# Kernel tuning notes

Measured on AMD Instinct MI355X. Metric: run time of the kernel, lower is better.

Reference implementation:

```python
import jax, jax.numpy as jnp
import numpy as np

LMAX = 6
BLOCK_SIZES = [(2 * l + 1) ** 2 for l in range(LMAX + 1)]  # [1,9,25,49,81,121,169], sum=455
IRREPS_DIM = sum(BLOCK_SIZES)


def setup_inputs() -> dict:
    key = jax.random.key(0)
    k1, k2, k3 = jax.random.split(key, 3)
    B, F_IN, F_OUT, N_GRID = 256, 128, 128, 512
    x = jax.random.normal(k1, (B, F_IN, IRREPS_DIM), dtype=jnp.float32)
    w = jax.random.normal(k2, (F_IN, F_OUT, N_GRID), dtype=jnp.float32)
    D = jax.random.normal(k3, (N_GRID, IRREPS_DIM), dtype=jnp.float32)
    return {"x": x, "w": w, "D": D}


def _so3_linear(x, psi):
    # x: [B, f_in, 455], psi: [f_in, f_out, 455]
    # Per-degree grouped linear: for each l, input block is (mul=2l+1, dim=2l+1),
    # weight block is (mul_in=2l+1, mul_out=2l+1); e3nn normalization 1/sqrt(f_in*mul_in).
    B, f_in, _ = x.shape
    f_out = psi.shape[1]
    outs = []
    off = 0
    for l in range(LMAX + 1):
        d = 2 * l + 1
        sz = d * d
        xb = x[:, :, off:off + sz].reshape(B, f_in, d, d)          # [B,f,u,i]
        wb = psi[:, :, off:off + sz].reshape(f_in, f_out, d, d)    # [f,g,u,v]
        yb = jnp.einsum('bfui,fguv->bgvi', xb, wb) / np.sqrt(f_in * d).astype(np.float32)
        outs.append(yb.reshape(B, f_out, sz))
        off += sz
    return jnp.concatenate(outs, axis=-1)  # [B, f_out, 455]


def reference(x, w, D):
    n_grid = D.shape[0]
    # Kernel synthesis from Wigner-D buffer: psi[f,g,i] = sum_n D[n,i] * w[f,g,n] / sqrt(n_grid)
    psi = jnp.einsum('ni,xyn->xyi', D, w) / np.float32(np.sqrt(n_grid))
    return _so3_linear(x, psi)
```

## Files before the change

### kernel.cpp

```cpp
#include <hip/hip_runtime.h>
#include <math.h>


typedef float f32x4 __attribute__((ext_vector_type(4)));
typedef short short8 __attribute__((ext_vector_type(8)));
typedef short short4v __attribute__((ext_vector_type(4)));
typedef __bf16 bf8 __attribute__((ext_vector_type(8)));

static __device__ inline bf8 as_bf8(short8 s) {
    union { short8 s; bf8 b; } u; u.s = s; return u.b;
}
static __device__ inline short f2bf(float f) {
    union { float f; unsigned u; } v; v.f = f;
    unsigned r = v.u + 0x7FFFu + ((v.u >> 16) & 1u);
    return (short)(r >> 16);
}
static __device__ __forceinline__ void glds16(const short* g, short* l) {
    __builtin_amdgcn_global_load_lds(
        (const __attribute__((address_space(1))) unsigned*)g,
        (__attribute__((address_space(3))) unsigned*)l, 16, 0, 0);
}

static const int OFFS_H[8] = {0, 1, 10, 35, 84, 165, 286, 455};
static const size_t PSIOFF_H[7] = {0, 16384, 163840, 573440, 1376256, 2703360, 4685824};
static const size_t XPOFF_H[7] = {0, 32768, 327680, 1146880, 2752512, 5406720, 9371648};
__constant__ int OFFS_D[8] = {0, 1, 10, 35, 84, 165, 286, 455};
__constant__ unsigned PSIOFF_D[7] = {0, 16384, 163840, 573440, 1376256, 2703360, 4685824};
__constant__ unsigned XPOFF_D[7] = {0, 32768, 327680, 1146880, 2752512, 5406720, 9371648};
__constant__ int PSTART2_D[7] = {0, 338, 580, 742, 840, 890, 908};

__global__ void transpose_D(const float* __restrict__ D, short* __restrict__ DT) {
    int idx = blockIdx.x * 256 + threadIdx.x;
    if (idx >= 455 * 512) return;
    int n = idx & 511, c = idx >> 9;
    DT[(size_t)c * 512 + n] = f2bf(D[(size_t)n * 455 + c]);
}

static __device__ __forceinline__ void psi_body(int rawid, const float* __restrict__ w,
                                                const short* __restrict__ DT,
                                                short* __restrict__ PSIall,
                                                short (*As)[72], short (*Bs)[72],
                                                int* colInfo) {
    int id = (rawid & 7) * 128 + (rawid >> 3);
    const int nt = id & 3, mt = id >> 2;
    const int tid = threadIdx.x, wave = tid >> 6, lane = tid & 63;
    const int wm = (wave & 1) * 32, wn = (wave >> 1) * 64;

    if (tid < 128) {
        int cp = nt * 128 + tid;
        int info = -1;
        if (cp < 455) {
            int l = 6;
            while (OFFS_D[l] > cp) --l;
            int t = cp - OFFS_D[l];
            int d = 2 * l + 1;
            int v = t / d, u = t - v * d;
            info = (OFFS_D[l] + u * d + v) | (u << 9) | (v << 13) | (l << 17);
        }
        colInfo[tid] = info;
    }
    __syncthreads();

    int brow[4];
#pragma unroll
    for (int c = 0; c < 4; ++c) {
        int inf = colInfo[(tid + c * 256) >> 3];
        brow[c] = (inf < 0) ? 0 : (inf & 511);
    }

    const float* Ag = w + (size_t)(mt * 64) * 512;
    f32x4 acc[2][4] = {};

    for (int k0 = 0; k0 < 512; k0 += 64) {
        __syncthreads();
#pragma unroll
        for (int c = 0; c < 4; ++c) {
            int e = (tid + c * 256) * 4;
            int r = e >> 6, cc = e & 63;
            float4 v = *reinterpret_cast<const float4*>(Ag + (size_t)r * 512 + k0 + cc);
            short4v s;
            s.x = f2bf(v.x); s.y = f2bf(v.y); s.z = f2bf(v.z); s.w = f2bf(v.w);
            *reinterpret_cast<short4v*>(&As[r][cc]) = s;
        }
#pragma unroll
        for (int c = 0; c < 4; ++c) {
            int ch = tid + c * 256;
            int r = ch >> 3, cc = (ch & 7) * 8;
            short8 v = *reinterpret_cast<const short8*>(DT + (size_t)brow[c] * 512 + k0 + cc);
            *reinterpret_cast<short8*>(&Bs[r][cc]) = v;
        }
        __syncthreads();
#pragma unroll
        for (int kf = 0; kf < 2; ++kf) {
            const int kc = kf * 32 + (lane >> 4) * 8;
            short8 af[2], bfr[4];
#pragma unroll
            for (int mi = 0; mi < 2; ++mi)
                af[mi] = *reinterpret_cast<const short8*>(&As[wm + mi * 16 + (lane & 15)][kc]);
#pragma unroll
            for (int ni = 0; ni < 4; ++ni)
                bfr[ni] = *reinterpret_cast<const short8*>(&Bs[wn + ni * 16 + (lane & 15)][kc]);
#pragma unroll
            for (int mi = 0; mi < 2; ++mi)
#pragma unroll
                for (int ni = 0; ni < 4; ++ni)
                    acc[mi][ni] = __builtin_amdgcn_mfma_f32_16x16x32_bf16(
                        as_bf8(af[mi]), as_bf8(bfr[ni]), acc[mi][ni], 0, 0, 0);
        }
    }

    const float s1 = 0.044194173824159216f;
    const int f = mt >> 1;
#pragma unroll
    for (int mi = 0; mi < 2; ++mi)
#pragma unroll
        for (int ni = 0; ni < 4; ++ni) {
            int inf = colInfo[wn + ni * 16 + (lane & 15)];
            if (inf >= 0) {
                int u = (inf >> 9) & 15, v = (inf >> 13) & 15, l = (inf >> 17) & 7;
                int d = 2 * l + 1;
                size_t base = PSIOFF_D[l];
#pragma unroll
                for (int r = 0; r < 4; ++r) {
                    int m = mt * 64 + wm + mi * 16 + (lane >> 4) * 4 + r;
                    int g = m & 127;
                    PSIall[base + (size_t)(g * d + v) * (128 * d) + f * d + u] =
                        f2bf(acc[mi][ni][r] * s1);
                }
            }
        }
}

static __device__ __forceinline__ void pack_body(int id, const float* __restrict__ x,
                                                 short* __restrict__ XPall,
                                                 short (*Ls)[170]) {
    const int l = 6 - (id >> 10);
    const int local = id & 1023;
    const int fc = local & 3, b = local >> 2;
    const int d = 2 * l + 1, sz = d * d, off = OFFS_D[l];
    const int K = 128 * d;

    const int tid = threadIdx.x;
    const float* xb = x + ((size_t)b * 128 + fc * 32) * 455 + off;
    const int total = 32 * sz;
    for (int e = tid; e < total; e += 256) {
        int ff = e / sz, t = e - ff * sz;
        Ls[ff][t] = f2bf(xb[(size_t)ff * 455 + t]);
    }
    __syncthreads();
    short* XP = XPall + XPOFF_D[l];
    const int row = 32 * d;
    for (int e = tid; e < total; e += 256) {
        int i = e / row;
        int rem = e - i * row;
        int ff = rem / d, u = rem - ff * d;
        XP[((size_t)b * d + i) * K + (fc * 32 + ff) * d + u] = Ls[ff][u * d + i];
    }
}

__global__ __launch_bounds__(256) void prep_all(const float* __restrict__ w,
                                                const short* __restrict__ DT,
                                                const float* __restrict__ x,
                                                short* __restrict__ PSIall,
                                                short* __restrict__ XPall) {
    __shared__ __align__(16) char smem[28160];
    const int bid = blockIdx.x;
    if (bid < 1024) {
        short (*As)[72] = (short(*)[72])smem;
        short (*Bs)[72] = (short(*)[72])(smem + 9216);
        int* colInfo = (int*)(smem + 27648);
        psi_body(bid, w, DT, PSIall, As, Bs, colInfo);
    } else {
        short (*Ls)[170] = (short(*)[170])smem;
        pack_body(bid - 1024, x, XPall, Ls);
    }
}

__global__ __launch_bounds__(256) void psi_gemm_all(const float* __restrict__ w,
                                                    const short* __restrict__ DT,
                                                    short* __restrict__ PSIall) {
    __shared__ short As[64][72];
    __shared__ short Bs[128][72];
    __shared__ int colInfo[128];
    psi_body(blockIdx.y * gridDim.x + blockIdx.x, w, DT, PSIall, As, Bs, colInfo);
}

template <int d>
__global__ __launch_bounds__(256) void pack_x(const float* __restrict__ x,
                                              short* __restrict__ XP, int off) {
    constexpr int sz = d * d;
    constexpr int K = 128 * d;
    const int fc = blockIdx.x, b = blockIdx.y;
    __shared__ short Ls[64][sz + 1];
    const int tid = threadIdx.x;
    const float* xb = x + ((size_t)b * 128 + fc * 64) * 455 + off;
    for (int e = tid; e < 64 * sz; e += 256) {
        int ff = e / sz, t = e - ff * sz;
        Ls[ff][t] = f2bf(xb[(size_t)ff * 455 + t]);
    }
    __syncthreads();
    for (int e = tid; e < 64 * sz; e += 256) {
        int i = e / (64 * d);
        int rem = e - i * (64 * d);
        int ff = rem / d, u = rem - ff * d;
        XP[((size_t)b * d + i) * K + (fc * 64 + ff) * d + u] = Ls[ff][u * d + i];
    }
}

template <int d>
__global__ __launch_bounds__(256) void psi_gemm(const float* __restrict__ w,
                                                const short* __restrict__ DT,
                                                short* __restrict__ PSI, int off) {
    constexpr int sz = d * d;
    constexpr int KP = 128 * d;
    const int mt = blockIdx.x;
    const int nt = blockIdx.y;
    const int tid = threadIdx.x, wave = tid >> 6, lane = tid & 63;
    const int wm = (wave & 1) * 32, wn = (wave >> 1) * 64;

    __shared__ short As[64][72];
    __shared__ short Bs[128][72];

    const float* Ag = w + (size_t)(mt * 64) * 512;
    f32x4 acc[2][4] = {};

    for (int k0 = 0; k0 < 512; k0 += 64) {
        __syncthreads();
#pragma unroll
        for (int c = 0; c < 4; ++c) {
            int e = (tid + c * 256) * 4;
            int r = e >> 6, cc = e & 63;
            float4 v = *reinterpret_cast<const float4*>(Ag + (size_t)r * 512 + k0 + cc);
            short4v s;
            s.x = f2bf(v.x); s.y = f2bf(v.y); s.z = f2bf(v.z); s.w = f2bf(v.w);
            *reinterpret_cast<short4v*>(&As[r][cc]) = s;
        }
#pragma unroll
        for (int c = 0; c < 4; ++c) {
            int ch = tid + c * 256;
            int r = ch >> 3, cc = (ch & 7) * 8;
            int gc = nt * 128 + r;
            int row = off + (gc < sz ? gc : 0);
            short8 v = *reinterpret_cast<const short8*>(DT + (size_t)row * 512 + k0 + cc);
            *reinterpret_cast<short8*>(&Bs[r][cc]) = v;
        }
        __syncthreads();
#pragma unroll
        for (int kf = 0; kf < 2; ++kf) {
            const int kc = kf * 32 + (lane >> 4) * 8;
            short8 af[2], bfr[4];
#pragma unroll
            for (int mi = 0; mi < 2; ++mi)
                af[mi] = *reinterpret_cast<const short8*>(&As[wm + mi * 16 + (lane & 15)][kc]);
#pragma unroll
            for (int ni = 0; ni < 4; ++ni)
                bfr[ni] = *reinterpret_cast<const short8*>(&Bs[wn + ni * 16 + (lane & 15)][kc]);
#pragma unroll
            for (int mi = 0; mi < 2; ++mi)
#pragma unroll
                for (int ni = 0; ni < 4; ++ni)
                    acc[mi][ni] = __builtin_amdgcn_mfma_f32_16x16x32_bf16(
                        as_bf8(af[mi]), as_bf8(bfr[ni]), acc[mi][ni], 0, 0, 0);
        }
    }

    const float s1 = 0.044194173824159216f;
#pragma unroll
    for (int mi = 0; mi < 2; ++mi)
#pragma unroll
        for (int ni = 0; ni < 4; ++ni) {
            int cix = nt * 128 + wn + ni * 16 + (lane & 15);
            if (cix < sz) {
                int u = cix / d, v = cix - u * d;
#pragma unroll
                for (int r = 0; r < 4; ++r) {
                    int m = mt * 64 + wm + mi * 16 + (lane >> 4) * 4 + r;
                    int f = m >> 7, g = m & 127;
                    PSI[(size_t)(g * d + v) * KP + f * d + u] = f2bf(acc[mi][ni][r] * s1);
                }
            }
        }
}

__global__ __launch_bounds__(256) void so3_gemm_all(const short* __restrict__ XPall,
                                                    const short* __restrict__ PSIall,
                                                    float* __restrict__ out) {
    const int p = blockIdx.x;
    int j = 6;
    while (PSTART2_D[j] > p) --j;
    const int l = 6 - j;
    const int d = 2 * l + 1;
    const int pp = p - PSTART2_D[j];
    const int S = 2 * d * d;
    const int q = S >> 3;
    const int xcd = pp & 7, pos = pp >> 3;
    const int local = (xcd < 2 ? xcd * (q + 1) : 2 * (q + 1) + (xcd - 2) * q) + pos;
    const int mt = local % d, nt = local / d;
    const int K = 128 * d;
    const int off = OFFS_D[l];

    const int tid = threadIdx.x, wave = tid >> 6, lane = tid & 63;
    const int wm = (wave & 1) * 64, wn = (wave >> 1) * 64;

    __shared__ short As[128 * 64];
    __shared__ short Bs[128 * 64];

    const short* Ag = PSIall + PSIOFF_D[l] + (size_t)(mt * 128) * K;
    const short* Bg = XPall + XPOFF_D[l] + (size_t)(nt * 128) * K;

    const int srow = wave * 32 + (lane >> 3);
    const int scol = (((lane & 7) ^ (lane >> 3)) << 3);
    f32x4 acc[4][4] = {};

    for (int k0 = 0; k0 < K; k0 += 64) {
        __syncthreads();
#pragma unroll
        for (int c = 0; c < 4; ++c)
            glds16(Ag + (size_t)(srow + 8 * c) * K + k0 + scol,
                   &As[(wave * 32 + 8 * c) * 64]);
#pragma unroll
        for (int c = 0; c < 4; ++c)
            glds16(Bg + (size_t)(srow + 8 * c) * K + k0 + scol,
                   &Bs[(wave * 32 + 8 * c) * 64]);
        __syncthreads();
#pragma unroll
        for (int kf = 0; kf < 2; ++kf) {
            const int so = (((kf * 4 + (lane >> 4)) ^ (lane & 7)) << 3);
            short8 af[4], bfr[4];
#pragma unroll
            for (int mi = 0; mi < 4; ++mi)
                af[mi] = *reinterpret_cast<const short8*>(
                    &As[(wm + mi * 16 + (lane & 15)) * 64 + so]);
#pragma unroll
            for (int ni = 0; ni < 4; ++ni)
                bfr[ni] = *reinterpret_cast<const short8*>(
                    &Bs[(wn + ni * 16 + (lane & 15)) * 64 + so]);
#pragma unroll
            for (int mi = 0; mi < 4; ++mi)
#pragma unroll
                for (int ni = 0; ni < 4; ++ni)
                    acc[mi][ni] = __builtin_amdgcn_mfma_f32_16x16x32_bf16(
                        as_bf8(af[mi]), as_bf8(bfr[ni]), acc[mi][ni], 0, 0, 0);
        }
    }

    const float s2 = rsqrtf(128.0f * (float)d);
#pragma unroll
    for (int mi = 0; mi < 4; ++mi)
#pragma unroll
        for (int ni = 0; ni < 4; ++ni) {
            int n = nt * 128 + wn + ni * 16 + (lane & 15);
            int b = n / d, i = n - b * d;
#pragma unroll
            for (int r = 0; r < 4; ++r) {
                int m = mt * 128 + wm + mi * 16 + (lane >> 4) * 4 + r;
                int g = m / d, v = m - g * d;
                out[((size_t)b * 128 + g) * 455 + off + v * d + i] = acc[mi][ni][r] * s2;
            }
        }
}

template <int d>
__global__ __launch_bounds__(256) void so3_gemm_fb(const short* __restrict__ XP,
                                                   const short* __restrict__ PSI,
                                                   float* __restrict__ out, int off) {
    constexpr int K = 128 * d;
    constexpr int GX = 2 * d;
    constexpr int NWG = 4 * d * d;
    int id = blockIdx.y * gridDim.x + blockIdx.x;
    {
        constexpr int q = NWG >> 3, rr = NWG & 7;
        int xcd = id & 7, pos = id >> 3;
        id = (xcd < rr ? xcd * (q + 1) : rr * (q + 1) + (xcd - rr) * q) + pos;
    }
    const int mt = id % GX, nt = id / GX;
    const int tid = threadIdx.x, wave = tid >> 6, lane = tid & 63;
    const int wm = (wave & 1) * 32, wn = (wave >> 1) * 64;

    __shared__ short As[64][72];
    __shared__ short Bs[128][72];

    const short* Ag = PSI + (size_t)(mt * 64) * K;
    const short* Bg = XP + (size_t)(nt * 128) * K;
    f32x4 acc[2][4] = {};

    for (int k0 = 0; k0 < K; k0 += 64) {
        __syncthreads();
#pragma unroll
        for (int c = 0; c < 2; ++c) {
            int ch = tid + c * 256;
            int r = ch >> 3, cc = (ch & 7) * 8;
            *reinterpret_cast<short8*>(&As[r][cc]) =
                *reinterpret_cast<const short8*>(Ag + (size_t)r * K + k0 + cc);
        }
#pragma unroll
        for (int c = 0; c < 4; ++c) {
            int ch = tid + c * 256;
            int r = ch >> 3, cc = (ch & 7) * 8;
            *reinterpret_cast<short8*>(&Bs[r][cc]) =
                *reinterpret_cast<const short8*>(Bg + (size_t)r * K + k0 + cc);
        }
        __syncthreads();
#pragma unroll
        for (int kf = 0; kf < 2; ++kf) {
            const int kc = kf * 32 + (lane >> 4) * 8;
            short8 af[2], bfr[4];
#pragma unroll
            for (int mi = 0; mi < 2; ++mi)
                af[mi] = *reinterpret_cast<const short8*>(&As[wm + mi * 16 + (lane & 15)][kc]);
#pragma unroll
            for (int ni = 0; ni < 4; ++ni)
                bfr[ni] = *reinterpret_cast<const short8*>(&Bs[wn + ni * 16 + (lane & 15)][kc]);
#pragma unroll
            for (int mi = 0; mi < 2; ++mi)
#pragma unroll
                for (int ni = 0; ni < 4; ++ni)
                    acc[mi][ni] = __builtin_amdgcn_mfma_f32_16x16x32_bf16(
                        as_bf8(af[mi]), as_bf8(bfr[ni]), acc[mi][ni], 0, 0, 0);
        }
    }

    const float s2 = rsqrtf(128.0f * (float)d);
#pragma unroll
    for (int mi = 0; mi < 2; ++mi)
#pragma unroll
        for (int ni = 0; ni < 4; ++ni) {
            int n = nt * 128 + wn + ni * 16 + (lane & 15);
            int b = n / d, i = n - b * d;
#pragma unroll
            for (int r = 0; r < 4; ++r) {
                int m = mt * 64 + wm + mi * 16 + (lane >> 4) * 4 + r;
                int g = m / d, v = m - g * d;
                out[((size_t)b * 128 + g) * 455 + off + v * d + i] = acc[mi][ni][r] * s2;
            }
        }
}

template <int l>
static void run_l_fb(const float* x, const float* w, const short* DT, short* PSIbase,
                     short* XP, float* out, bool fused, hipStream_t stream) {
    constexpr int d = 2 * l + 1;
    const int off = OFFS_H[l];
    if (!fused) {
        constexpr int sz = d * d;
        constexpr int ntiles = (sz + 127) / 128;
        psi_gemm<d><<<dim3(256, ntiles), 256, 0, stream>>>(w, DT, PSIbase, off);
    }
    pack_x<d><<<dim3(2, 256), 256, 0, stream>>>(x, XP, off);
    const short* P = fused ? (PSIbase + PSIOFF_H[l]) : PSIbase;
    so3_gemm_fb<d><<<dim3(2 * d, 2 * d), 256, 0, stream>>>(XP, P, out, off);
}

extern "C" void kernel_launch(void* const* d_in, const int* in_sizes, int n_in,
                              void* d_out, int out_size, void* d_ws, size_t ws_size,
                              hipStream_t stream) {
    const float* x = (const float*)d_in[0];
    const float* w = (const float*)d_in[1];
    const float* D = (const float*)d_in[2];
    float* out = (float*)d_out;

    char* ws = (char*)d_ws;
    const size_t dtBytes      = (size_t)455 * 512 * 2;
    const size_t psiAllBytes  = (size_t)7454720 * 2;
    const size_t psiSlotBytes = (size_t)1664 * 1664 * 2;
    const size_t xpL6Bytes    = (size_t)3328 * 1664 * 2;
    const size_t xpAllBytes   = (size_t)14909440 * 2;

    short* DT = (short*)ws;
    transpose_D<<<(455 * 512 + 255) / 256, 256, 0, stream>>>(D, DT);

    if (ws_size >= dtBytes + psiAllBytes + xpAllBytes) {
        short* PSIall = (short*)(ws + dtBytes);
        short* XPall  = (short*)(ws + dtBytes + psiAllBytes);
        prep_all<<<dim3(8192), 256, 0, stream>>>(w, DT, x, PSIall, XPall);
        so3_gemm_all<<<dim3(910), 256, 0, stream>>>(XPall, PSIall, out);
        return;
    }

    const bool fused = ws_size >= dtBytes + psiAllBytes + xpL6Bytes;
    short* PSIbase = (short*)(ws + dtBytes);
    short* XP = (short*)(ws + dtBytes + (fused ? psiAllBytes : psiSlotBytes));
    if (fused)
        psi_gemm_all<<<dim3(4, 256), 256, 0, stream>>>(w, DT, PSIbase);

    run_l_fb<0>(x, w, DT, PSIbase, XP, out, fused, stream);
    run_l_fb<1>(x, w, DT, PSIbase, XP, out, fused, stream);
    run_l_fb<2>(x, w, DT, PSIbase, XP, out, fused, stream);
    run_l_fb<3>(x, w, DT, PSIbase, XP, out, fused, stream);
    run_l_fb<4>(x, w, DT, PSIbase, XP, out, fused, stream);
    run_l_fb<5>(x, w, DT, PSIbase, XP, out, fused, stream);
    run_l_fb<6>(x, w, DT, PSIbase, XP, out, fused, stream);
}
```

Baseline: 136.2 us.

## Halve GEMM M-tile to 64 and double-buffer LDS loads in so3_gemm_all

The grouped GEMM tile shrinks from 128x128 to 64x128, doubling the workgroup count from 910 to 1820 so more blocks are available to fill the CUs. The LDS buffers become double-buffered: the next K-slice's global-to-LDS loads are issued before computing on the current slice, with one barrier per iteration instead of two. In exchange, each block gets half the MFMA work per B-tile load, so B traffic goes up, and the XCD remapping constants change to match the new grid.

```diff
diff --git a/kernel.cpp b/kernel.cpp
--- a/kernel.cpp
+++ b/kernel.cpp
@@ -27,7 +27,7 @@
 __constant__ int OFFS_D[8] = {0, 1, 10, 35, 84, 165, 286, 455};
 __constant__ unsigned PSIOFF_D[7] = {0, 16384, 163840, 573440, 1376256, 2703360, 4685824};
 __constant__ unsigned XPOFF_D[7] = {0, 32768, 327680, 1146880, 2752512, 5406720, 9371648};
-__constant__ int PSTART2_D[7] = {0, 338, 580, 742, 840, 890, 908};
+__constant__ int PSTART_D[7] = {0, 676, 1160, 1484, 1680, 1780, 1816};
 
 __global__ void transpose_D(const float* __restrict__ D, short* __restrict__ DT) {
     int idx = blockIdx.x * 256 + threadIdx.x;
@@ -287,73 +287,94 @@
                                                     float* __restrict__ out) {
     const int p = blockIdx.x;
     int j = 6;
-    while (PSTART2_D[j] > p) --j;
+    while (PSTART_D[j] > p) --j;
     const int l = 6 - j;
     const int d = 2 * l + 1;
-    const int pp = p - PSTART2_D[j];
-    const int S = 2 * d * d;
+    const int pp = p - PSTART_D[j];
+    const int S = 4 * d * d;
     const int q = S >> 3;
     const int xcd = pp & 7, pos = pp >> 3;
-    const int local = (xcd < 2 ? xcd * (q + 1) : 2 * (q + 1) + (xcd - 2) * q) + pos;
-    const int mt = local % d, nt = local / d;
+    const int local = (xcd < 4 ? xcd * (q + 1) : 4 * (q + 1) + (xcd - 4) * q) + pos;
+    const int mtiles = 2 * d;
+    const int mt = local % mtiles, nt = local / mtiles;
     const int K = 128 * d;
+    const int NT = K >> 6;
     const int off = OFFS_D[l];
 
     const int tid = threadIdx.x, wave = tid >> 6, lane = tid & 63;
-    const int wm = (wave & 1) * 64, wn = (wave >> 1) * 64;
-
-    __shared__ short As[128 * 64];
-    __shared__ short Bs[128 * 64];
-
-    const short* Ag = PSIall + PSIOFF_D[l] + (size_t)(mt * 128) * K;
+    const int wm = (wave & 1) * 32, wn = (wave >> 1) * 64;
+
+    __shared__ short As[2][64 * 64];
+    __shared__ short Bs[2][128 * 64];
+
+    const short* Ag = PSIall + PSIOFF_D[l] + (size_t)(mt * 64) * K;
     const short* Bg = XPall + XPOFF_D[l] + (size_t)(nt * 128) * K;
 
-    const int srow = wave * 32 + (lane >> 3);
-    const int scol = (((lane & 7) ^ (lane >> 3)) << 3);
-    f32x4 acc[4][4] = {};
-
-    for (int k0 = 0; k0 < K; k0 += 64) {
-        __syncthreads();
-#pragma unroll
-        for (int c = 0; c < 4; ++c)
-            glds16(Ag + (size_t)(srow + 8 * c) * K + k0 + scol,
-                   &As[(wave * 32 + 8 * c) * 64]);
-#pragma unroll
-        for (int c = 0; c < 4; ++c)
-            glds16(Bg + (size_t)(srow + 8 * c) * K + k0 + scol,
-                   &Bs[(wave * 32 + 8 * c) * 64]);
-        __syncthreads();
+    const int lrow = lane >> 3;
+    const int scol = (((lane & 7) ^ lrow) << 3);
+
+    f32x4 acc[2][4] = {};
+
+#pragma unroll
+    for (int c = 0; c < 2; ++c)
+        glds16(Ag + (size_t)(wave * 16 + 8 * c + lrow) * K + scol,
+               &As[0][(wave * 16 + 8 * c) * 64]);
+#pragma unroll
+    for (int c = 0; c < 4; ++c)
+        glds16(Bg + (size_t)(wave * 32 + 8 * c + lrow) * K + scol,
+               &Bs[0][(wave * 32 + 8 * c) * 64]);
+    __syncthreads();
+
+    int cur = 0;
+    for (int t = 0; t < NT; ++t) {
+        if (t + 1 < NT) {
+            const int k0n = (t + 1) * 64;
+            short* An = As[cur ^ 1];
+            short* Bn = Bs[cur ^ 1];
+#pragma unroll
+            for (int c = 0; c < 2; ++c)
+                glds16(Ag + (size_t)(wave * 16 + 8 * c + lrow) * K + k0n + scol,
+                       &An[(wave * 16 + 8 * c) * 64]);
+#pragma unroll
+            for (int c = 0; c < 4; ++c)
+                glds16(Bg + (size_t)(wave * 32 + 8 * c + lrow) * K + k0n + scol,
+                       &Bn[(wave * 32 + 8 * c) * 64]);
+        }
+        const short* Ac = As[cur];
+        const short* Bc = Bs[cur];
 #pragma unroll
         for (int kf = 0; kf < 2; ++kf) {
             const int so = (((kf * 4 + (lane >> 4)) ^ (lane & 7)) << 3);
-            short8 af[4], bfr[4];
-#pragma unroll
-            for (int mi = 0; mi < 4; ++mi)
+            short8 af[2], bfr[4];
+#pragma unroll
+            for (int mi = 0; mi < 2; ++mi)
                 af[mi] = *reinterpret_cast<const short8*>(
-                    &As[(wm + mi * 16 + (lane & 15)) * 64 + so]);
+                    &Ac[(wm + mi * 16 + (lane & 15)) * 64 + so]);
 #pragma unroll
             for (int ni = 0; ni < 4; ++ni)
                 bfr[ni] = *reinterpret_cast<const short8*>(
-                    &Bs[(wn + ni * 16 + (lane & 15)) * 64 + so]);
-#pragma unroll
-            for (int mi = 0; mi < 4; ++mi)
+                    &Bc[(wn + ni * 16 + (lane & 15)) * 64 + so]);
+#pragma unroll
+            for (int mi = 0; mi < 2; ++mi)
 #pragma unroll
                 for (int ni = 0; ni < 4; ++ni)
                     acc[mi][ni] = __builtin_amdgcn_mfma_f32_16x16x32_bf16(
                         as_bf8(af[mi]), as_bf8(bfr[ni]), acc[mi][ni], 0, 0, 0);
         }
+        __syncthreads();
+        cur ^= 1;
     }
 
     const float s2 = rsqrtf(128.0f * (float)d);
 #pragma unroll
-    for (int mi = 0; mi < 4; ++mi)
+    for (int mi = 0; mi < 2; ++mi)
 #pragma unroll
         for (int ni = 0; ni < 4; ++ni) {
             int n = nt * 128 + wn + ni * 16 + (lane & 15);
             int b = n / d, i = n - b * d;
 #pragma unroll
             for (int r = 0; r < 4; ++r) {
-                int m = mt * 128 + wm + mi * 16 + (lane >> 4) * 4 + r;
+                int m = mt * 64 + wm + mi * 16 + (lane >> 4) * 4 + r;
                 int g = m / d, v = m - g * d;
                 out[((size_t)b * 128 + g) * 455 + off + v * d + i] = acc[mi][ni][r] * s2;
             }
@@ -473,7 +494,7 @@
         short* PSIall = (short*)(ws + dtBytes);
         short* XPall  = (short*)(ws + dtBytes + psiAllBytes);
         prep_all<<<dim3(8192), 256, 0, stream>>>(w, DT, x, PSIall, XPall);
-        so3_gemm_all<<<dim3(910), 256, 0, stream>>>(XPall, PSIall, out);
+        so3_gemm_all<<<dim3(1820), 256, 0, stream>>>(XPall, PSIall, out);
         return;
     }
 
```

New measurement: 139.0 us. 2.0% more time.
